# Performance work log

Hardware: AMD Instinct MI355X
Metric: run time of the kernel (lower is better)

## Reference

```python
import jax, jax.numpy as jnp
import numpy as np

EPS = 1e-12

def l2norm(x, axis):
    # torch.nn.functional.normalize: x / max(||x||_2, eps)
    n = jnp.sqrt(jnp.sum(x * x, axis=axis, keepdims=True))
    return x / jnp.maximum(n, EPS)

def setup_inputs() -> dict:
    key = jax.random.key(0)
    k1, k2, k3, k4 = jax.random.split(key, 4)
    B, Cf, H, W = 128, 1024, 16, 16
    n_att, dv = 312, 300
    img = jax.random.normal(k1, (B, Cf, H, W), dtype=jnp.float32)
    # V is initialized from row-normalized w2v embeddings in the module
    V = l2norm(jax.random.normal(k2, (n_att, dv), dtype=jnp.float32), axis=1)
    W1 = jax.random.normal(k3, (dv, Cf), dtype=jnp.float32)
    W2 = jax.random.normal(k4, (dv, Cf), dtype=jnp.float32)
    return {"img": img, "V": V, "W1": W1, "W2": W2}

def reference(img, V, W1, W2):
    vv = l2norm(V, axis=1)                               # [i, v]
    B, Cf, H, Wd = img.shape
    av = l2norm(img.reshape(B, Cf, H * Wd), axis=1)      # [b, f, r]
    Q = vv @ W1                                          # [i, f]
    A = jnp.einsum('if,bfr->bir', Q, av)                 # attention logits
    A = jax.nn.softmax(A, axis=-1)
    F_p = jnp.einsum('bir,bfr->bif', A, av)              # attended features
    Pred_att = jnp.einsum('if,bif->bi', vv @ W2, F_p)
    return Pred_att
```

## Files before the change

### kernel.cpp

```cpp
#include <hip/hip_runtime.h>
#include <math.h>

#define NB   128
#define CF   1024
#define RR   256
#define NA   312
#define DV   300
#define M2   320
#define MT   640
#define NKC  32
#define NQ   160

typedef _Float16 half8  __attribute__((ext_vector_type(8)));
typedef _Float16 half4  __attribute__((ext_vector_type(4)));
typedef float float16v  __attribute__((ext_vector_type(16)));
typedef float float4v   __attribute__((ext_vector_type(4)));

__device__ __forceinline__ void gll16(const void* g, void* l) {
    __builtin_amdgcn_global_load_lds(
        (const __attribute__((address_space(1))) void*)g,
        (__attribute__((address_space(3))) void*)l, 16, 0, 0);
}

__launch_bounds__(256, 6)
__global__ void k_pq(const float* __restrict__ img, float* __restrict__ ssq32,
                     _Float16* __restrict__ avT,
                     const float* __restrict__ V, const float* __restrict__ W1,
                     const float* __restrict__ W2, _Float16* __restrict__ Qb) {
    int lin = blockIdx.x;
    int t = threadIdx.x;
    if (lin >= NQ) {
        int m  = lin - NQ;
        int kc = m & 31;
        int b  = m >> 5;
        int kk8 = t & 3;
        int rq  = t >> 2;
        const float* src = img + ((size_t)b * CF + kc * 32 + kk8 * 8) * RR + rq * 4;
        float4v v[8];
        #pragma unroll
        for (int j = 0; j < 8; ++j) v[j] = *(const float4v*)(src + (size_t)j * RR);
        float ss0 = 0.f, ss1 = 0.f, ss2 = 0.f, ss3 = 0.f;
        #pragma unroll
        for (int j = 0; j < 8; ++j) {
            ss0 += v[j][0] * v[j][0]; ss1 += v[j][1] * v[j][1];
            ss2 += v[j][2] * v[j][2]; ss3 += v[j][3] * v[j][3];
        }
        _Float16* dst = avT + ((size_t)(b * NKC + kc) * RR + rq * 4) * 32 + kk8 * 8;
        #pragma unroll
        for (int s = 0; s < 4; ++s) {
            half8 o;
            #pragma unroll
            for (int j = 0; j < 8; ++j) o[j] = (_Float16)v[j][s];
            *(half8*)(dst + (size_t)s * 32) = o;
        }
        ss0 += __shfl_xor(ss0, 1, 64); ss0 += __shfl_xor(ss0, 2, 64);
        ss1 += __shfl_xor(ss1, 1, 64); ss1 += __shfl_xor(ss1, 2, 64);
        ss2 += __shfl_xor(ss2, 1, 64); ss2 += __shfl_xor(ss2, 2, 64);
        ss3 += __shfl_xor(ss3, 1, 64); ss3 += __shfl_xor(ss3, 2, 64);
        if (kk8 == 0) {
            float4v sv; sv[0] = ss0; sv[1] = ss1; sv[2] = ss2; sv[3] = ss3;
            *(float4v*)(ssq32 + ((size_t)b * NKC + kc) * RR + rq * 4) = sv;
        }
    } else {
        int ib = lin;
        bool isQ2 = ib >= 80;
        int i0l = (ib - (isQ2 ? 80 : 0)) * 4;
        int i0g = (isQ2 ? M2 : 0) + i0l;
        __shared__ float inv4[4];
        float acc[4][4];
        #pragma unroll
        for (int ii = 0; ii < 4; ++ii)
            #pragma unroll
            for (int j = 0; j < 4; ++j) acc[ii][j] = 0.f;
        if (i0l < NA) {
            int row = t >> 6, l64 = t & 63;
            float s = 0.f;
            for (int v = l64; v < DV; v += 64) { float x = V[(i0l + row) * DV + v]; s += x * x; }
            #pragma unroll
            for (int o = 32; o; o >>= 1) s += __shfl_xor(s, o, 64);
            if (l64 == 0) inv4[row] = 1.f / fmaxf(sqrtf(s), 1e-12f);
            __syncthreads();
            const float* W  = isQ2 ? W2 : W1;
            const float* Vb = V + (size_t)i0l * DV;
            for (int v = 0; v < DV; v += 2) {
                float4v w0 = *(const float4v*)(W + (size_t)v * CF + t * 4);
                float4v w1 = *(const float4v*)(W + (size_t)(v + 1) * CF + t * 4);
                #pragma unroll
                for (int ii = 0; ii < 4; ++ii) {
                    float a0 = Vb[(size_t)ii * DV + v];
                    float a1 = Vb[(size_t)ii * DV + v + 1];
                    #pragma unroll
                    for (int j = 0; j < 4; ++j) acc[ii][j] += a0 * w0[j] + a1 * w1[j];
                }
            }
            #pragma unroll
            for (int ii = 0; ii < 4; ++ii)
                #pragma unroll
                for (int j = 0; j < 4; ++j) acc[ii][j] *= inv4[ii];
        }
        int fg = t >> 3;
        int fo = (t & 7) * 4;
        #pragma unroll
        for (int ii = 0; ii < 4; ++ii) {
            half4 h;
            #pragma unroll
            for (int j = 0; j < 4; ++j) h[j] = (_Float16)acc[ii][j];
            *(half4*)&Qb[((size_t)fg * MT + (i0g + ii)) * 32 + fo] = h;
        }
    }
}

__launch_bounds__(256, 3)
__global__ void k_gemm(const _Float16* __restrict__ Qb, const _Float16* __restrict__ avT,
                       const float* __restrict__ ssq32, float* __restrict__ out) {
    int lin  = blockIdx.x;
    int xcd  = lin & 7;
    int slot = lin >> 3;
    int bq   = slot / 5;
    int t2   = slot - bq * 5;
    int b    = bq * 8 + xcd;

    int tid = threadIdx.x;
    int lane = tid & 63, w = tid >> 6;
    int nl = lane & 31, kh = lane >> 5;

    __shared__ __align__(16) char smem[49152];
    _Float16* A0 = (_Float16*)smem;
    _Float16* A1 = (_Float16*)(smem + 8192);
    _Float16* B0 = (_Float16*)(smem + 16384);
    _Float16* B1 = (_Float16*)(smem + 32768);
    float* mred = (float*)smem;
    float* mg   = (float*)(smem + 1024);
    float* sred = (float*)(smem + 1280);
    float* dred = (float*)(smem + 2304);

    float16v acc[4][2];
    #pragma unroll
    for (int i = 0; i < 4; ++i)
        #pragma unroll
        for (int j = 0; j < 2; ++j)
            #pragma unroll
            for (int gi = 0; gi < 16; ++gi) acc[i][j][gi] = 0.f;

    int arow  = tid & 127;
    int akb0  = tid >> 7;
    int grow  = (arow < 64) ? (t2 * 64 + arow) : (M2 + t2 * 64 + (arow - 64));
    size_t a_src0 = (size_t)grow * 32 + akb0 * 8;
    const _Float16* bpanel = avT + (size_t)b * NKC * RR * 32;

    #define STAGE(kc_, Ab, Bb) do {                                                  \
        const _Float16* as_ = Qb + (size_t)(kc_) * MT * 32 + a_src0;                 \
        gll16(as_,      (char*)(Ab) + tid * 16);                                     \
        gll16(as_ + 16, (char*)(Ab) + tid * 16 + 4096);                              \
        const _Float16* bs_ = bpanel + (size_t)(kc_) * RR * 32 + (size_t)tid * 32;   \
        gll16(bs_,      (char*)(Bb) + tid * 16);                                     \
        gll16(bs_ + 8,  (char*)(Bb) + tid * 16 + 4096);                              \
        gll16(bs_ + 16, (char*)(Bb) + tid * 16 + 8192);                              \
        gll16(bs_ + 24, (char*)(Bb) + tid * 16 + 12288);                             \
    } while (0)

    #define COMPUTE(Al, Bl) do {                                                     \
        _Pragma("unroll")                                                            \
        for (int ks = 0; ks < 2; ++ks) {                                             \
            int kb = ks * 2 + kh;                                                    \
            half8 b0f = *(const half8*)((Bl) + ((size_t)kb * 256 + w * 64 + nl) * 8);       \
            half8 b1f = *(const half8*)((Bl) + ((size_t)kb * 256 + w * 64 + 32 + nl) * 8);  \
            _Pragma("unroll")                                                        \
            for (int rf = 0; rf < 4; ++rf) {                                         \
                half8 af = *(const half8*)((Al) + ((size_t)kb * 128 + rf * 32 + nl) * 8);   \
                acc[rf][0] = __builtin_amdgcn_mfma_f32_32x32x16_f16(af, b0f, acc[rf][0], 0, 0, 0); \
                acc[rf][1] = __builtin_amdgcn_mfma_f32_32x32x16_f16(af, b1f, acc[rf][1], 0, 0, 0); \
            }                                                                        \
        }                                                                            \
    } while (0)

    STAGE(0, A0, B0);
    STAGE(1, A1, B1);
    asm volatile("s_waitcnt vmcnt(6)" ::: "memory");
    __builtin_amdgcn_s_barrier();
    __builtin_amdgcn_sched_barrier(0);

    #pragma unroll 1
    for (int kc = 0; kc < NKC - 2; kc += 2) {
        COMPUTE(A0, B0);
        __builtin_amdgcn_s_barrier();
        __builtin_amdgcn_sched_barrier(0);
        STAGE(kc + 2, A0, B0);
        asm volatile("s_waitcnt vmcnt(6)" ::: "memory");
        __builtin_amdgcn_s_barrier();
        __builtin_amdgcn_sched_barrier(0);
        COMPUTE(A1, B1);
        __builtin_amdgcn_s_barrier();
        __builtin_amdgcn_sched_barrier(0);
        STAGE(kc + 3, A1, B1);
        asm volatile("s_waitcnt vmcnt(6)" ::: "memory");
        __builtin_amdgcn_s_barrier();
        __builtin_amdgcn_sched_barrier(0);
    }
    COMPUTE(A0, B0);
    asm volatile("s_waitcnt vmcnt(0)" ::: "memory");
    __builtin_amdgcn_s_barrier();
    __builtin_amdgcn_sched_barrier(0);
    COMPUTE(A1, B1);

    #undef STAGE
    #undef COMPUTE

    const float* sq = ssq32 + (size_t)b * NKC * RR;
    int c0 = w * 64 + nl;
    float p0 = 0.f, p1 = 0.f;
    #pragma unroll
    for (int kc = 0; kc < NKC; ++kc) {
        p0 += sq[(size_t)kc * RR + c0];
        p1 += sq[(size_t)kc * RR + 32 + c0];
    }
    float iv0 = 1.f / fmaxf(sqrtf(p0), 1e-12f);
    float iv1 = 1.f / fmaxf(sqrtf(p1), 1e-12f);
    #pragma unroll
    for (int rf = 0; rf < 4; ++rf)
        #pragma unroll
        for (int gi = 0; gi < 16; ++gi) {
            acc[rf][0][gi] *= iv0;
            acc[rf][1][gi] *= iv1;
        }

    float mx[2][16];
    #pragma unroll
    for (int p = 0; p < 2; ++p)
        #pragma unroll
        for (int gi = 0; gi < 16; ++gi)
            mx[p][gi] = fmaxf(acc[p][0][gi], acc[p][1][gi]);
    #pragma unroll
    for (int off = 1; off <= 16; off <<= 1)
        #pragma unroll
        for (int p = 0; p < 2; ++p)
            #pragma unroll
            for (int gi = 0; gi < 16; ++gi)
                mx[p][gi] = fmaxf(mx[p][gi], __shfl_xor(mx[p][gi], off, 64));
    if (nl == 0) {
        #pragma unroll
        for (int p = 0; p < 2; ++p)
            #pragma unroll
            for (int gi = 0; gi < 16; ++gi) {
                int row = (gi & 3) + 8 * (gi >> 2) + 4 * kh;
                mred[(p * 32 + row) * 4 + w] = mx[p][gi];
            }
    }
    __syncthreads();
    if (tid < 64)
        mg[tid] = fmaxf(fmaxf(mred[tid * 4], mred[tid * 4 + 1]),
                        fmaxf(mred[tid * 4 + 2], mred[tid * 4 + 3]));
    __syncthreads();
    float sp[2][16], dp[2][16];
    #pragma unroll
    for (int p = 0; p < 2; ++p)
        #pragma unroll
        for (int gi = 0; gi < 16; ++gi) {
            int row = (gi & 3) + 8 * (gi >> 2) + 4 * kh;
            float m  = mg[p * 32 + row];
            float e0 = __expf(acc[p][0][gi] - m);
            float e1 = __expf(acc[p][1][gi] - m);
            sp[p][gi] = e0 + e1;
            dp[p][gi] = e0 * acc[p + 2][0][gi] + e1 * acc[p + 2][1][gi];
        }
    #pragma unroll
    for (int off = 1; off <= 16; off <<= 1)
        #pragma unroll
        for (int p = 0; p < 2; ++p)
            #pragma unroll
            for (int gi = 0; gi < 16; ++gi) {
                sp[p][gi] += __shfl_xor(sp[p][gi], off, 64);
                dp[p][gi] += __shfl_xor(dp[p][gi], off, 64);
            }
    if (nl == 0) {
        #pragma unroll
        for (int p = 0; p < 2; ++p)
            #pragma unroll
            for (int gi = 0; gi < 16; ++gi) {
                int row = (gi & 3) + 8 * (gi >> 2) + 4 * kh;
                sred[(p * 32 + row) * 4 + w] = sp[p][gi];
                dred[(p * 32 + row) * 4 + w] = dp[p][gi];
            }
    }
    __syncthreads();
    if (tid < 64) {
        float s = sred[tid * 4] + sred[tid * 4 + 1] + sred[tid * 4 + 2] + sred[tid * 4 + 3];
        float d = dred[tid * 4] + dred[tid * 4 + 1] + dred[tid * 4 + 2] + dred[tid * 4 + 3];
        int ig = t2 * 64 + tid;
        if (ig < NA) out[b * NA + ig] = d / s;
    }
}

extern "C" void kernel_launch(void* const* d_in, const int* in_sizes, int n_in,
                              void* d_out, int out_size, void* d_ws, size_t ws_size,
                              hipStream_t stream) {
    const float* img = (const float*)d_in[0];
    const float* V   = (const float*)d_in[1];
    const float* W1  = (const float*)d_in[2];
    const float* W2  = (const float*)d_in[3];
    float* out = (float*)d_out;

    char* ws = (char*)d_ws;
    size_t off = 0;
    float*    ssq32 = (float*)(ws + off);    off += (size_t)NB * NKC * RR * 4;
    _Float16* avT   = (_Float16*)(ws + off); off += (size_t)NB * CF * RR * 2;
    _Float16* Qb    = (_Float16*)(ws + off); off += (size_t)NKC * MT * 32 * 2;

    k_pq<<<dim3(NQ + NB * NKC), 256, 0, stream>>>(img, ssq32, avT, V, W1, W2, Qb);
    k_gemm<<<dim3(640), 256, 0, stream>>>(Qb, avT, ssq32, out);
}
```

Baseline: 307.6 us.

## Enlarge gemm tile to 320 rows, interleave Q1/Q2, triple-buffer with 512 threads

Q1 and Q2 rows are now interleaved in the Qb layout, so each softmax row's logit and value columns land in adjacent accumulator elements. The gemm block grows to 512 threads computing 320 (interleaved) rows by 256 columns per batch, launched as 256 blocks instead of 640. The K loop changes from double to triple buffering using 108 KB of dynamic LDS. The intent is fewer redundant loads of the image panel and better MFMA reuse. The cost is fewer resident blocks per CU and a larger LDS footprint.

```diff
diff --git a/kernel.cpp b/kernel.cpp
--- a/kernel.cpp
+++ b/kernel.cpp
@@ -6,7 +6,6 @@
 #define RR   256
 #define NA   312
 #define DV   300
-#define M2   320
 #define MT   640
 #define NKC  32
 #define NQ   160
@@ -65,7 +64,6 @@
         int ib = lin;
         bool isQ2 = ib >= 80;
         int i0l = (ib - (isQ2 ? 80 : 0)) * 4;
-        int i0g = (isQ2 ? M2 : 0) + i0l;
         __shared__ float inv4[4];
         float acc[4][4];
         #pragma unroll
@@ -100,193 +98,182 @@
         }
         int fg = t >> 3;
         int fo = (t & 7) * 4;
+        int q12 = isQ2 ? 1 : 0;
         #pragma unroll
         for (int ii = 0; ii < 4; ++ii) {
             half4 h;
             #pragma unroll
             for (int j = 0; j < 4; ++j) h[j] = (_Float16)acc[ii][j];
-            *(half4*)&Qb[((size_t)fg * MT + (i0g + ii)) * 32 + fo] = h;
+            *(half4*)&Qb[((size_t)fg * MT + (2 * (i0l + ii) + q12)) * 32 + fo] = h;
         }
     }
 }
 
-__launch_bounds__(256, 3)
+extern __shared__ char smem[];
+__launch_bounds__(512, 2)
 __global__ void k_gemm(const _Float16* __restrict__ Qb, const _Float16* __restrict__ avT,
                        const float* __restrict__ ssq32, float* __restrict__ out) {
-    int lin  = blockIdx.x;
-    int xcd  = lin & 7;
-    int slot = lin >> 3;
-    int bq   = slot / 5;
-    int t2   = slot - bq * 5;
-    int b    = bq * 8 + xcd;
-
-    int tid = threadIdx.x;
-    int lane = tid & 63, w = tid >> 6;
-    int nl = lane & 31, kh = lane >> 5;
-
-    __shared__ __align__(16) char smem[49152];
-    _Float16* A0 = (_Float16*)smem;
-    _Float16* A1 = (_Float16*)(smem + 8192);
-    _Float16* B0 = (_Float16*)(smem + 16384);
-    _Float16* B1 = (_Float16*)(smem + 32768);
-    float* mred = (float*)smem;
-    float* mg   = (float*)(smem + 1024);
-    float* sred = (float*)(smem + 1280);
-    float* dred = (float*)(smem + 2304);
-
-    float16v acc[4][2];
-    #pragma unroll
-    for (int i = 0; i < 4; ++i)
+    int lin = blockIdx.x;
+    int xcd = lin & 7;
+    int u   = lin >> 3;
+    int b   = xcd + 8 * (u & 15);
+    int t2h = u >> 4;
+
+    int tid  = threadIdx.x;
+    int lane = tid & 63;
+    int w    = tid >> 6;
+    int wm   = w >> 2;
+    int wn   = w & 3;
+    int nl   = lane & 31;
+    int kh   = lane >> 5;
+
+    int c1 = 512 + tid;
+    int a_s0 = (tid % 320) * 64 + (tid / 320) * 16;
+    int a_s1 = (c1 % 320) * 64 + (c1 / 320) * 16;
+    int a_s2 = ((tid & 255) + 64) * 64 + 3 * 16;
+    int a_d0 = tid * 16;
+    int a_d1 = a_d0 + 8192;
+    int a_d2 = 16384 + (tid & 255) * 16;
+    int b_s0 = (tid & 255) * 64 + (tid >> 8) * 16;
+
+    const char* Abase_g = (const char*)Qb;
+    const char* Bbase_g = (const char*)avT + ((size_t)b * NKC) * RR * 64;
+
+    float16v acc[5][2];
+    #pragma unroll
+    for (int i = 0; i < 5; ++i)
         #pragma unroll
         for (int j = 0; j < 2; ++j)
             #pragma unroll
             for (int gi = 0; gi < 16; ++gi) acc[i][j][gi] = 0.f;
 
-    int arow  = tid & 127;
-    int akb0  = tid >> 7;
-    int grow  = (arow < 64) ? (t2 * 64 + arow) : (M2 + t2 * 64 + (arow - 64));
-    size_t a_src0 = (size_t)grow * 32 + akb0 * 8;
-    const _Float16* bpanel = avT + (size_t)b * NKC * RR * 32;
-
-    #define STAGE(kc_, Ab, Bb) do {                                                  \
-        const _Float16* as_ = Qb + (size_t)(kc_) * MT * 32 + a_src0;                 \
-        gll16(as_,      (char*)(Ab) + tid * 16);                                     \
-        gll16(as_ + 16, (char*)(Ab) + tid * 16 + 4096);                              \
-        const _Float16* bs_ = bpanel + (size_t)(kc_) * RR * 32 + (size_t)tid * 32;   \
-        gll16(bs_,      (char*)(Bb) + tid * 16);                                     \
-        gll16(bs_ + 8,  (char*)(Bb) + tid * 16 + 4096);                              \
-        gll16(bs_ + 16, (char*)(Bb) + tid * 16 + 8192);                              \
-        gll16(bs_ + 24, (char*)(Bb) + tid * 16 + 12288);                             \
+    char* p0 = smem;
+    char* p1 = smem + 36864;
+    char* p2 = smem + 73728;
+
+    #define STAGE(kc_, buf) do {                                                   \
+        int kcl = (kc_) < NKC ? (kc_) : (NKC - 1);                                 \
+        const char* aS = Abase_g + ((size_t)kcl * MT + (size_t)t2h * 320) * 64;    \
+        const char* bS = Bbase_g + (size_t)kcl * RR * 64;                          \
+        char* ab = (buf); char* bb = (buf) + 20480;                                \
+        gll16(aS + a_s0, ab + a_d0);                                               \
+        gll16(aS + a_s1, ab + a_d1);                                               \
+        gll16(aS + a_s2, ab + a_d2);                                               \
+        gll16(bS + b_s0,      bb + tid * 16);                                      \
+        gll16(bS + b_s0 + 32, bb + tid * 16 + 8192);                               \
     } while (0)
 
-    #define COMPUTE(Al, Bl) do {                                                     \
-        _Pragma("unroll")                                                            \
-        for (int ks = 0; ks < 2; ++ks) {                                             \
-            int kb = ks * 2 + kh;                                                    \
-            half8 b0f = *(const half8*)((Bl) + ((size_t)kb * 256 + w * 64 + nl) * 8);       \
-            half8 b1f = *(const half8*)((Bl) + ((size_t)kb * 256 + w * 64 + 32 + nl) * 8);  \
-            _Pragma("unroll")                                                        \
-            for (int rf = 0; rf < 4; ++rf) {                                         \
-                half8 af = *(const half8*)((Al) + ((size_t)kb * 128 + rf * 32 + nl) * 8);   \
-                acc[rf][0] = __builtin_amdgcn_mfma_f32_32x32x16_f16(af, b0f, acc[rf][0], 0, 0, 0); \
-                acc[rf][1] = __builtin_amdgcn_mfma_f32_32x32x16_f16(af, b1f, acc[rf][1], 0, 0, 0); \
-            }                                                                        \
-        }                                                                            \
+    #define COMPUTE(buf) do {                                                      \
+        const char* Al = (buf); const char* Bl = (buf) + 20480;                    \
+        _Pragma("unroll")                                                          \
+        for (int ks = 0; ks < 2; ++ks) {                                           \
+            int kb = ks * 2 + kh;                                                  \
+            half8 bf0 = *(const half8*)(Bl + ((size_t)kb * 256 + wn * 64 + nl) * 16);      \
+            half8 bf1 = *(const half8*)(Bl + ((size_t)kb * 256 + wn * 64 + 32 + nl) * 16); \
+            _Pragma("unroll")                                                      \
+            for (int mt = 0; mt < 5; ++mt) {                                       \
+                half8 af = *(const half8*)(Al + ((size_t)kb * 320 + wm * 160 + mt * 32 + nl) * 16); \
+                acc[mt][0] = __builtin_amdgcn_mfma_f32_32x32x16_f16(af, bf0, acc[mt][0], 0, 0, 0);  \
+                acc[mt][1] = __builtin_amdgcn_mfma_f32_32x32x16_f16(af, bf1, acc[mt][1], 0, 0, 0);  \
+            }                                                                      \
+        }                                                                          \
     } while (0)
 
-    STAGE(0, A0, B0);
-    STAGE(1, A1, B1);
-    asm volatile("s_waitcnt vmcnt(6)" ::: "memory");
+    STAGE(0, p0);
+    __builtin_amdgcn_sched_barrier(0);
+    STAGE(1, p1);
+    asm volatile("s_waitcnt vmcnt(5)" ::: "memory");
     __builtin_amdgcn_s_barrier();
     __builtin_amdgcn_sched_barrier(0);
 
     #pragma unroll 1
-    for (int kc = 0; kc < NKC - 2; kc += 2) {
-        COMPUTE(A0, B0);
+    for (int kc = 0; kc < NKC; ++kc) {
+        STAGE(kc + 2, p2);
+        asm volatile("s_waitcnt vmcnt(5)" ::: "memory");
+        __builtin_amdgcn_sched_barrier(0);
+        COMPUTE(p0);
+        __builtin_amdgcn_sched_barrier(0);
         __builtin_amdgcn_s_barrier();
-        __builtin_amdgcn_sched_barrier(0);
-        STAGE(kc + 2, A0, B0);
-        asm volatile("s_waitcnt vmcnt(6)" ::: "memory");
-        __builtin_amdgcn_s_barrier();
-        __builtin_amdgcn_sched_barrier(0);
-        COMPUTE(A1, B1);
-        __builtin_amdgcn_s_barrier();
-        __builtin_amdgcn_sched_barrier(0);
-        STAGE(kc + 3, A1, B1);
-        asm volatile("s_waitcnt vmcnt(6)" ::: "memory");
-        __builtin_amdgcn_s_barrier();
-        __builtin_amdgcn_sched_barrier(0);
-    }
-    COMPUTE(A0, B0);
+        char* tmp = p0; p0 = p1; p1 = p2; p2 = tmp;
+    }
     asm volatile("s_waitcnt vmcnt(0)" ::: "memory");
     __builtin_amdgcn_s_barrier();
     __builtin_amdgcn_sched_barrier(0);
-    COMPUTE(A1, B1);
-
     #undef STAGE
     #undef COMPUTE
 
+    float* mred = (float*)smem;
+    float* mg   = (float*)(smem + 2560);
+    float* sred = (float*)(smem + 3200);
+    float* dred = (float*)(smem + 5760);
+
     const float* sq = ssq32 + (size_t)b * NKC * RR;
-    int c0 = w * 64 + nl;
-    float p0 = 0.f, p1 = 0.f;
+    int c0 = wn * 64 + nl;
+    float q0 = 0.f, q1 = 0.f;
     #pragma unroll
     for (int kc = 0; kc < NKC; ++kc) {
-        p0 += sq[(size_t)kc * RR + c0];
-        p1 += sq[(size_t)kc * RR + 32 + c0];
-    }
-    float iv0 = 1.f / fmaxf(sqrtf(p0), 1e-12f);
-    float iv1 = 1.f / fmaxf(sqrtf(p1), 1e-12f);
-    #pragma unroll
-    for (int rf = 0; rf < 4; ++rf)
+        q0 += sq[(size_t)kc * RR + c0];
+        q1 += sq[(size_t)kc * RR + 32 + c0];
+    }
+    float iv0 = 1.f / fmaxf(sqrtf(q0), 1e-12f);
+    float iv1 = 1.f / fmaxf(sqrtf(q1), 1e-12f);
+    #pragma unroll
+    for (int mt = 0; mt < 5; ++mt)
         #pragma unroll
         for (int gi = 0; gi < 16; ++gi) {
-            acc[rf][0][gi] *= iv0;
-            acc[rf][1][gi] *= iv1;
-        }
-
-    float mx[2][16];
-    #pragma unroll
-    for (int p = 0; p < 2; ++p)
-        #pragma unroll
-        for (int gi = 0; gi < 16; ++gi)
-            mx[p][gi] = fmaxf(acc[p][0][gi], acc[p][1][gi]);
-    #pragma unroll
-    for (int off = 1; off <= 16; off <<= 1)
-        #pragma unroll
-        for (int p = 0; p < 2; ++p)
-            #pragma unroll
-            for (int gi = 0; gi < 16; ++gi)
-                mx[p][gi] = fmaxf(mx[p][gi], __shfl_xor(mx[p][gi], off, 64));
-    if (nl == 0) {
-        #pragma unroll
-        for (int p = 0; p < 2; ++p)
-            #pragma unroll
-            for (int gi = 0; gi < 16; ++gi) {
-                int row = (gi & 3) + 8 * (gi >> 2) + 4 * kh;
-                mred[(p * 32 + row) * 4 + w] = mx[p][gi];
+            acc[mt][0][gi] *= iv0;
+            acc[mt][1][gi] *= iv1;
+        }
+
+    #pragma unroll
+    for (int mt = 0; mt < 5; ++mt) {
+        #pragma unroll
+        for (int e = 0; e < 8; ++e) {
+            int g = 2 * e;
+            float mx = fmaxf(acc[mt][0][g], acc[mt][1][g]);
+            #pragma unroll
+            for (int off = 1; off <= 16; off <<= 1)
+                mx = fmaxf(mx, __shfl_xor(mx, off, 64));
+            if (nl == 0) {
+                int row = (g & 3) + 8 * (g >> 2) + 4 * kh;
+                mred[wn * 160 + wm * 80 + mt * 16 + (row >> 1)] = mx;
             }
+        }
     }
     __syncthreads();
-    if (tid < 64)
-        mg[tid] = fmaxf(fmaxf(mred[tid * 4], mred[tid * 4 + 1]),
-                        fmaxf(mred[tid * 4 + 2], mred[tid * 4 + 3]));
+    if (tid < 160)
+        mg[tid] = fmaxf(fmaxf(mred[tid], mred[160 + tid]),
+                        fmaxf(mred[320 + tid], mred[480 + tid]));
     __syncthreads();
-    float sp[2][16], dp[2][16];
-    #pragma unroll
-    for (int p = 0; p < 2; ++p)
-        #pragma unroll
-        for (int gi = 0; gi < 16; ++gi) {
-            int row = (gi & 3) + 8 * (gi >> 2) + 4 * kh;
-            float m  = mg[p * 32 + row];
-            float e0 = __expf(acc[p][0][gi] - m);
-            float e1 = __expf(acc[p][1][gi] - m);
-            sp[p][gi] = e0 + e1;
-            dp[p][gi] = e0 * acc[p + 2][0][gi] + e1 * acc[p + 2][1][gi];
-        }
-    #pragma unroll
-    for (int off = 1; off <= 16; off <<= 1)
-        #pragma unroll
-        for (int p = 0; p < 2; ++p)
-            #pragma unroll
-            for (int gi = 0; gi < 16; ++gi) {
-                sp[p][gi] += __shfl_xor(sp[p][gi], off, 64);
-                dp[p][gi] += __shfl_xor(dp[p][gi], off, 64);
+
+    #pragma unroll
+    for (int mt = 0; mt < 5; ++mt) {
+        #pragma unroll
+        for (int e = 0; e < 8; ++e) {
+            int g = 2 * e;
+            int row = (g & 3) + 8 * (g >> 2) + 4 * kh;
+            int Pl = wm * 80 + mt * 16 + (row >> 1);
+            float m = mg[Pl];
+            float e0 = __expf(acc[mt][0][g] - m);
+            float e1 = __expf(acc[mt][1][g] - m);
+            float s = e0 + e1;
+            float d = e0 * acc[mt][0][g + 1] + e1 * acc[mt][1][g + 1];
+            #pragma unroll
+            for (int off = 1; off <= 16; off <<= 1) {
+                s += __shfl_xor(s, off, 64);
+                d += __shfl_xor(d, off, 64);
             }
-    if (nl == 0) {
-        #pragma unroll
-        for (int p = 0; p < 2; ++p)
-            #pragma unroll
-            for (int gi = 0; gi < 16; ++gi) {
-                int row = (gi & 3) + 8 * (gi >> 2) + 4 * kh;
-                sred[(p * 32 + row) * 4 + w] = sp[p][gi];
-                dred[(p * 32 + row) * 4 + w] = dp[p][gi];
+            if (nl == 0) {
+                sred[wn * 160 + Pl] = s;
+                dred[wn * 160 + Pl] = d;
             }
+        }
     }
     __syncthreads();
-    if (tid < 64) {
-        float s = sred[tid * 4] + sred[tid * 4 + 1] + sred[tid * 4 + 2] + sred[tid * 4 + 3];
-        float d = dred[tid * 4] + dred[tid * 4 + 1] + dred[tid * 4 + 2] + dred[tid * 4 + 3];
-        int ig = t2 * 64 + tid;
+    if (tid < 160) {
+        float s = sred[tid] + sred[160 + tid] + sred[320 + tid] + sred[480 + tid];
+        float d = dred[tid] + dred[160 + tid] + dred[320 + tid] + dred[480 + tid];
+        int ig = t2h * 160 + tid;
         if (ig < NA) out[b * NA + ig] = d / s;
     }
 }
@@ -306,6 +293,13 @@
     _Float16* avT   = (_Float16*)(ws + off); off += (size_t)NB * CF * RR * 2;
     _Float16* Qb    = (_Float16*)(ws + off); off += (size_t)NKC * MT * 32 * 2;
 
+    static bool attr_done = false;
+    if (!attr_done) {
+        hipFuncSetAttribute((const void*)k_gemm,
+                            hipFuncAttributeMaxDynamicSharedMemorySize, 110592);
+        attr_done = true;
+    }
+
     k_pq<<<dim3(NQ + NB * NKC), 256, 0, stream>>>(img, ssq32, avT, V, W1, W2, Qb);
-    k_gemm<<<dim3(640), 256, 0, stream>>>(Qb, avT, ssq32, out);
+    k_gemm<<<dim3(256), 512, 110592, stream>>>(Qb, avT, ssq32, out);
 }
```

Result: faster. 283.2 us (-7.9%).

## Stage image tile through LDS for transpose and restructure Q projection

Applied to the files above, without the earlier changes.

The normalization/transpose branch now loads each 32x256 image slab into shared memory with direct global-to-LDS loads. Each thread then reads one spatial column of 32 features, so the squared-norm reduction no longer needs cross-lane shuffles. The Q-projection branch switches to scalar per-feature W loads over four feature chunks. It leaves behind a leftover accumulation loop that is unused. Launch bounds are lowered for both kernels and an extra barrier is added after the GEMM main loop, trading occupancy for register headroom.

```diff
diff --git a/kernel.cpp b/kernel.cpp
--- a/kernel.cpp
+++ b/kernel.cpp
@@ -12,7 +12,6 @@
 #define NQ   160
 
 typedef _Float16 half8  __attribute__((ext_vector_type(8)));
-typedef _Float16 half4  __attribute__((ext_vector_type(4)));
 typedef float float16v  __attribute__((ext_vector_type(16)));
 typedef float float4v   __attribute__((ext_vector_type(4)));
 
@@ -22,57 +21,53 @@
         (__attribute__((address_space(3))) void*)l, 16, 0, 0);
 }
 
-__launch_bounds__(256, 6)
+__launch_bounds__(256, 4)
 __global__ void k_pq(const float* __restrict__ img, float* __restrict__ ssq32,
                      _Float16* __restrict__ avT,
                      const float* __restrict__ V, const float* __restrict__ W1,
                      const float* __restrict__ W2, _Float16* __restrict__ Qb) {
+    __shared__ __align__(16) char smem_s[32768];
     int lin = blockIdx.x;
     int t = threadIdx.x;
     if (lin >= NQ) {
         int m  = lin - NQ;
         int kc = m & 31;
         int b  = m >> 5;
-        int kk8 = t & 3;
-        int rq  = t >> 2;
-        const float* src = img + ((size_t)b * CF + kc * 32 + kk8 * 8) * RR + rq * 4;
-        float4v v[8];
-        #pragma unroll
-        for (int j = 0; j < 8; ++j) v[j] = *(const float4v*)(src + (size_t)j * RR);
-        float ss0 = 0.f, ss1 = 0.f, ss2 = 0.f, ss3 = 0.f;
-        #pragma unroll
-        for (int j = 0; j < 8; ++j) {
-            ss0 += v[j][0] * v[j][0]; ss1 += v[j][1] * v[j][1];
-            ss2 += v[j][2] * v[j][2]; ss3 += v[j][3] * v[j][3];
-        }
-        _Float16* dst = avT + ((size_t)(b * NKC + kc) * RR + rq * 4) * 32 + kk8 * 8;
+        float (*tile)[256] = (float (*)[256])smem_s;
+
+        const char* src = (const char*)(img + ((size_t)b * CF + kc * 32) * RR);
+        #pragma unroll
+        for (int i = 0; i < 8; ++i)
+            gll16(src + (size_t)i * 4096 + (size_t)t * 16,
+                  smem_s + i * 4096 + t * 16);
+        asm volatile("s_waitcnt vmcnt(0)" ::: "memory");
+        __syncthreads();
+
+        float v[32];
+        #pragma unroll
+        for (int f = 0; f < 32; ++f) v[f] = tile[f][t];
+        float ss = 0.f;
+        #pragma unroll
+        for (int f = 0; f < 32; ++f) ss += v[f] * v[f];
+
+        _Float16* dst = avT + ((size_t)(b * NKC + kc) * RR + t) * 32;
         #pragma unroll
         for (int s = 0; s < 4; ++s) {
             half8 o;
             #pragma unroll
-            for (int j = 0; j < 8; ++j) o[j] = (_Float16)v[j][s];
-            *(half8*)(dst + (size_t)s * 32) = o;
-        }
-        ss0 += __shfl_xor(ss0, 1, 64); ss0 += __shfl_xor(ss0, 2, 64);
-        ss1 += __shfl_xor(ss1, 1, 64); ss1 += __shfl_xor(ss1, 2, 64);
-        ss2 += __shfl_xor(ss2, 1, 64); ss2 += __shfl_xor(ss2, 2, 64);
-        ss3 += __shfl_xor(ss3, 1, 64); ss3 += __shfl_xor(ss3, 2, 64);
-        if (kk8 == 0) {
-            float4v sv; sv[0] = ss0; sv[1] = ss1; sv[2] = ss2; sv[3] = ss3;
-            *(float4v*)(ssq32 + ((size_t)b * NKC + kc) * RR + rq * 4) = sv;
-        }
+            for (int j = 0; j < 8; ++j) o[j] = (_Float16)v[s * 8 + j];
+            *(half8*)(dst + s * 8) = o;
+        }
+        ssq32[(size_t)(b * NKC + kc) * RR + t] = ss;
     } else {
         int ib = lin;
+        float* inv4 = (float*)smem_s;
         bool isQ2 = ib >= 80;
         int i0l = (ib - (isQ2 ? 80 : 0)) * 4;
         int i0g = (isQ2 ? M2 : 0) + i0l;
-        __shared__ float inv4[4];
-        float acc[4][4];
-        #pragma unroll
-        for (int ii = 0; ii < 4; ++ii)
-            #pragma unroll
-            for (int j = 0; j < 4; ++j) acc[ii][j] = 0.f;
-        if (i0l < NA) {
+        float acc[4] = {0, 0, 0, 0};
+        bool zero = (i0l >= NA);
+        if (!zero) {
             int row = t >> 6, l64 = t & 63;
             float s = 0.f;
             for (int v = l64; v < DV; v += 64) { float x = V[(i0l + row) * DV + v]; s += x * x; }
@@ -80,37 +75,46 @@
             for (int o = 32; o; o >>= 1) s += __shfl_xor(s, o, 64);
             if (l64 == 0) inv4[row] = 1.f / fmaxf(sqrtf(s), 1e-12f);
             __syncthreads();
-            const float* W  = isQ2 ? W2 : W1;
-            const float* Vb = V + (size_t)i0l * DV;
-            for (int v = 0; v < DV; v += 2) {
-                float4v w0 = *(const float4v*)(W + (size_t)v * CF + t * 4);
-                float4v w1 = *(const float4v*)(W + (size_t)(v + 1) * CF + t * 4);
+            const float* W = isQ2 ? W2 : W1;
+            for (int v = 0; v < DV; v += 4) {
+                float w0 = W[(size_t)(v + 0) * CF + t];
+                float w1 = W[(size_t)(v + 1) * CF + t];
+                float w2 = W[(size_t)(v + 2) * CF + t];
+                float w3 = W[(size_t)(v + 3) * CF + t];
                 #pragma unroll
                 for (int ii = 0; ii < 4; ++ii) {
-                    float a0 = Vb[(size_t)ii * DV + v];
-                    float a1 = Vb[(size_t)ii * DV + v + 1];
+                    const float* Vr = V + (size_t)(i0l + ii) * DV + v;
+                    acc[ii] += Vr[0] * w0 + Vr[1] * w1 + Vr[2] * w2 + Vr[3] * w3;
+                }
+            }
+        }
+        for (int fc = 0; fc < 4; ++fc) {
+            int f = fc * 256 + t;
+            float a4[4] = {0, 0, 0, 0};
+            if (!zero) {
+                const float* W = isQ2 ? W2 : W1;
+                for (int v = 0; v < DV; v += 4) {
+                    float w0 = W[(size_t)(v + 0) * CF + f];
+                    float w1 = W[(size_t)(v + 1) * CF + f];
+                    float w2 = W[(size_t)(v + 2) * CF + f];
+                    float w3 = W[(size_t)(v + 3) * CF + f];
                     #pragma unroll
-                    for (int j = 0; j < 4; ++j) acc[ii][j] += a0 * w0[j] + a1 * w1[j];
+                    for (int ii = 0; ii < 4; ++ii) {
+                        const float* Vr = V + (size_t)(i0l + ii) * DV + v;
+                        a4[ii] += Vr[0] * w0 + Vr[1] * w1 + Vr[2] * w2 + Vr[3] * w3;
+                    }
                 }
+                #pragma unroll
+                for (int ii = 0; ii < 4; ++ii) a4[ii] *= inv4[ii];
             }
             #pragma unroll
             for (int ii = 0; ii < 4; ++ii)
-                #pragma unroll
-                for (int j = 0; j < 4; ++j) acc[ii][j] *= inv4[ii];
-        }
-        int fg = t >> 3;
-        int fo = (t & 7) * 4;
-        #pragma unroll
-        for (int ii = 0; ii < 4; ++ii) {
-            half4 h;
-            #pragma unroll
-            for (int j = 0; j < 4; ++j) h[j] = (_Float16)acc[ii][j];
-            *(half4*)&Qb[((size_t)fg * MT + (i0g + ii)) * 32 + fo] = h;
+                Qb[((size_t)(f >> 5) * MT + (i0g + ii)) * 32 + (f & 31)] = (_Float16)a4[ii];
         }
     }
 }
 
-__launch_bounds__(256, 3)
+__launch_bounds__(256, 2)
 __global__ void k_gemm(const _Float16* __restrict__ Qb, const _Float16* __restrict__ avT,
                        const float* __restrict__ ssq32, float* __restrict__ out) {
     int lin  = blockIdx.x;
@@ -202,6 +206,7 @@
     __builtin_amdgcn_s_barrier();
     __builtin_amdgcn_sched_barrier(0);
     COMPUTE(A1, B1);
+    __builtin_amdgcn_s_barrier();
 
     #undef STAGE
     #undef COMPUTE
```

New measurement: 318.7 us. 1.04x slower.
